# Kernel tuning notes

Hardware: AMD Instinct MI355X
Metric: run time of the kernel (lower is better)

Reference implementation:

```python
import jax, jax.numpy as jnp
import numpy as np
from jax import lax

E = 300      # embed == hidden size
EN_V = 5967  # english vocab
ZH_V = 12016 # chinese vocab
B = 64
S = 64       # max_seq_len


def setup_inputs():
    key = jax.random.key(0)
    ks = jax.random.split(key, 12)
    sc = 1.0 / np.sqrt(E)

    def rn(k, shape):
        return jax.random.normal(k, shape, jnp.float32) * sc

    return {
        "en_input": jax.random.randint(ks[0], (B, S), 0, EN_V),
        "zh_input": jax.random.randint(ks[1], (B, S), 0, ZH_V),
        "en_embed": rn(ks[2], (EN_V, E)),
        "zh_embed": rn(ks[3], (ZH_V, E)),
        "enc_Wih": rn(ks[4], (2, 4 * E, E)),   # layer-stacked, PyTorch gate order i,f,g,o
        "enc_Whh": rn(ks[5], (2, 4 * E, E)),
        "enc_b": rn(ks[6], (2, 4 * E)),        # b_ih + b_hh fused (mathematically identical)
        "dec_Wih": rn(ks[7], (2, 4 * E, E)),
        "dec_Whh": rn(ks[8], (2, 4 * E, E)),
        "dec_b": rn(ks[9], (2, 4 * E)),
        "fc_W": rn(ks[10], (ZH_V, E)),
        "fc_b": rn(ks[11], (ZH_V,)),
    }


def _lstm_layer(x, h0, c0, Wih, Whh, b):
    # x: [B, T, Din]. PyTorch gate order: input, forget, cell(g), output.
    def step(carry, xt):
        h, c = carry
        gates = xt @ Wih.T + h @ Whh.T + b  # [B, 4H]
        i, f, g, o = jnp.split(gates, 4, axis=-1)
        c = jax.nn.sigmoid(f) * c + jax.nn.sigmoid(i) * jnp.tanh(g)
        h = jax.nn.sigmoid(o) * jnp.tanh(c)
        return (h, c), h

    (hT, cT), hs = lax.scan(step, (h0, c0), jnp.swapaxes(x, 0, 1))
    return jnp.swapaxes(hs, 0, 1), hT, cT  # [B,T,H], [B,H], [B,H]


def _lstm2(x, h0, c0, Wih, Whh, b):
    # 2-layer stacked LSTM (dropout between layers disabled: eval-mode math).
    hs, cs = [], []
    out = x
    for l in range(2):
        out, hT, cT = _lstm_layer(out, h0[l], c0[l], Wih[l], Whh[l], b[l])
        hs.append(hT)
        cs.append(cT)
    return out, jnp.stack(hs), jnp.stack(cs)


def reference(en_input, zh_input, en_embed, zh_embed, enc_Wih, enc_Whh, enc_b,
              dec_Wih, dec_Whh, dec_b, fc_W, fc_b):
    zh_feed, zh_target = zh_input[:, :-1], zh_input[:, 1:]
    b = en_input.shape[0]
    z = jnp.zeros((2, b, E), jnp.float32)

    # Encoder over source embeddings; final (h, c) seeds the decoder.
    _, h, c = _lstm2(en_embed[en_input], z, z, enc_Wih, enc_Whh, enc_b)

    # With teaching=True the per-step decoder loop is exactly a full-sequence LSTM.
    dec_out, _, _ = _lstm2(zh_embed[zh_feed], h, c, dec_Wih, dec_Whh, dec_b)

    logits = dec_out @ fc_W.T + fc_b          # [B, S-1, ZH_V]
    log_probs = jax.nn.log_softmax(logits, axis=2)

    # NLL loss with ignore_index=0 (mean over non-pad targets).
    mask = (zh_target != 0).astype(jnp.float32)
    picked = jnp.take_along_axis(log_probs, zh_target[:, :, None], axis=2)[:, :, 0]
    loss = -(picked * mask).sum() / mask.sum()
    return log_probs, loss
```

## Files before the change

kernel.cpp:

```cpp
#include <hip/hip_runtime.h>
#include <stdint.h>

#define EDIM   300
#define EPAD   304
#define KPAD   320
#define NG     1200
#define NB     64
#define SENC   64
#define SDEC   63
#define ZHV    12016
#define DROWS  4032
#define MPAD   4096
#define SENT   0xFFC0ACDCu
#define GSLOT  (NB*NG)

typedef unsigned short u16;
typedef __attribute__((ext_vector_type(8))) short bf16x8;
typedef __attribute__((ext_vector_type(4))) float f32x4;

static __device__ __forceinline__ float bflo(uint32_t u){ return __builtin_bit_cast(float, u << 16); }
static __device__ __forceinline__ float bfhi(uint32_t u){ return __builtin_bit_cast(float, u & 0xffff0000u); }
static __device__ __forceinline__ u16 f2bf(float f){
  uint32_t u = __builtin_bit_cast(uint32_t, f);
  return (u16)((u + 0x7fffu + ((u >> 16) & 1u)) >> 16);
}
static __device__ __forceinline__ float sigm(float x){ return 1.f/(1.f + __expf(-x)); }
static __device__ __forceinline__ float tanhf_(float x){
  x = fminf(fmaxf(x, -15.f), 15.f);
  float e = __expf(2.f*x);
  return (e - 1.f)/(e + 1.f);
}

__global__ void zero_kernel(float4* p, long n){
  long i = (long)blockIdx.x*blockDim.x + threadIdx.x;
  long st = (long)gridDim.x*blockDim.x;
  float4 z = {0.f,0.f,0.f,0.f};
  for (; i < n; i += st) p[i] = z;
}
__global__ void fill_sent(uint32_t* p, long n){
  long i = (long)blockIdx.x*blockDim.x + threadIdx.x;
  long st = (long)gridDim.x*blockDim.x;
  for (; i < n; i += st) p[i] = SENT;
}

__global__ void build_whh(const float* __restrict__ W, u16* __restrict__ out){
  int idx = blockIdx.x*blockDim.x + threadIdx.x;
  if (idx >= 20*38*64) return;
  int jl = idx & 63;
  int kc = (idx >> 6) % 38;
  int g  = (idx >> 6) / 38;
  int G = g/5, w = g - G*5;
  int jg = w*64 + jl;
  union { u16 u[8]; uint4 q; } v;
  for (int e=0;e<8;e++){
    int k = kc*8+e;
    float f = (jg < EDIM && k < EDIM) ? W[(size_t)(G*EDIM + jg)*EDIM + k] : 0.f;
    v.u[e] = f2bf(f);
  }
  ((uint4*)out)[idx] = v.q;
}

__global__ void build_b(const float* __restrict__ W, u16* __restrict__ out, int N){
  int idx = blockIdx.x*blockDim.x + threadIdx.x;
  if (idx >= N*EDIM) return;
  int n = idx / EDIM, k = idx - n*EDIM;
  out[(size_t)n*KPAD + k] = f2bf(W[idx]);
}

__global__ void embed_en(const int* __restrict__ ids, const float* __restrict__ emb, u16* __restrict__ x){
  int idx = blockIdx.x*blockDim.x + threadIdx.x;
  if (idx >= MPAD*EDIM) return;
  int r = idx / EDIM, k = idx - r*EDIM;
  x[(size_t)r*KPAD + k] = f2bf(emb[(size_t)ids[r]*EDIM + k]);
}
__global__ void embed_zh(const int* __restrict__ zh, const float* __restrict__ emb, u16* __restrict__ x){
  int idx = blockIdx.x*blockDim.x + threadIdx.x;
  if (idx >= DROWS*EDIM) return;
  int r = idx / EDIM, k = idx - r*EDIM;
  int b = r / SDEC, t = r - b*SDEC;
  x[(size_t)r*KPAD + k] = f2bf(emb[(size_t)zh[b*SENC + t]*EDIM + k]);
}

#define LDT 40
__global__ __launch_bounds__(256) void gemm_nt(const u16* __restrict__ A, const u16* __restrict__ B,
                float* __restrict__ C, int ldc, int Mreal, int Nreal, const float* __restrict__ bias){
  __shared__ __align__(16) u16 As[128*LDT];
  __shared__ __align__(16) u16 Bs[128*LDT];
  int tid = threadIdx.x;
  int lane = tid & 63, wave = tid >> 6;
  int wm = wave >> 1, wn = wave & 1;
  int m0 = blockIdx.y*128, n0 = blockIdx.x*128;
  f32x4 acc[4][4];
  for (int i=0;i<4;i++) for (int j=0;j<4;j++) acc[i][j] = (f32x4){0.f,0.f,0.f,0.f};
  int r16 = lane & 15, kg = lane >> 4;
  for (int kt=0; kt<KPAD/32; kt++){
    int k0 = kt*32;
    for (int c=0;c<2;c++){
      int id = c*256 + tid;
      int row = id >> 2, col = id & 3;
      *(uint4*)&As[row*LDT + col*8] = *(const uint4*)&A[(size_t)(m0+row)*KPAD + k0 + col*8];
      *(uint4*)&Bs[row*LDT + col*8] = *(const uint4*)&B[(size_t)(n0+row)*KPAD + k0 + col*8];
    }
    __syncthreads();
    bf16x8 af[4], bfr[4];
    for (int i=0;i<4;i++) af[i]  = *(const bf16x8*)&As[(wm*64 + i*16 + r16)*LDT + kg*8];
    for (int j=0;j<4;j++) bfr[j] = *(const bf16x8*)&Bs[(wn*64 + j*16 + r16)*LDT + kg*8];
    for (int i=0;i<4;i++)
      for (int j=0;j<4;j++)
        acc[i][j] = __builtin_amdgcn_mfma_f32_16x16x32_bf16(af[i], bfr[j], acc[i][j], 0, 0, 0);
    __syncthreads();
  }
  for (int j=0;j<4;j++){
    int col = n0 + wn*64 + j*16 + r16;
    if (col >= Nreal) continue;
    float bv = bias ? bias[col] : 0.f;
    for (int i=0;i<4;i++){
      int rbase = m0 + wm*64 + i*16 + kg*4;
      for (int r=0;r<4;r++){
        int row = rbase + r;
        if (row < Mreal) C[(size_t)row*ldc + col] = acc[i][j][r] + bv;
      }
    }
  }
}

__global__ __launch_bounds__(320) void recur_kernel(
    const float* __restrict__ Xih, const u16* __restrict__ Wt,
    const float* __restrict__ bias, const float* __restrict__ h0,
    const float* __restrict__ c0, float* gx,
    u16* seq, float* hfin, float* cfin, int steps)
{
  int r = blockIdx.x >> 2, G = blockIdx.x & 3;
  int tid = threadIdx.x;
  __shared__ __align__(16) float h_lds[EPAD];
  bool act = tid < EDIM;
  int jj = tid;
  int w = jj >> 6, jl = jj & 63;
  int g0 = G*5 + w;
  const uint4* wt4 = (const uint4*)Wt;
  int wbase = g0*38*64 + jl;
  float bj = act ? bias[G*EDIM + jj] : 0.f;
  float c_reg = act ? c0[r*EDIM + tid] : 0.f;
  if (tid < EDIM) h_lds[tid] = h0[r*EDIM + tid];
  else if (tid < EPAD) h_lds[tid] = 0.f;
  __syncthreads();
  int slice0 = G*75;
  for (int t=0; t<steps; t++){
    if (act){
      float xv = Xih[(size_t)(r*steps + t)*NG + G*EDIM + jj];
      float a0=0.f, a1=0.f, a2=0.f, a3=0.f;
      #pragma unroll
      for (int kc=0; kc<38; kc++){
        uint4 wv = wt4[wbase + (kc<<6)];
        float4 hA = *(const float4*)&h_lds[kc*8];
        float4 hB = *(const float4*)&h_lds[kc*8+4];
        a0 += hA.x*bflo(wv.x); a1 += hA.y*bfhi(wv.x);
        a2 += hA.z*bflo(wv.y); a3 += hA.w*bfhi(wv.y);
        a0 += hB.x*bflo(wv.z); a1 += hB.y*bfhi(wv.z);
        a2 += hB.z*bflo(wv.w); a3 += hB.w*bfhi(wv.w);
      }
      float acc = bj + xv + ((a0+a1) + (a2+a3));
      __hip_atomic_store(&gx[(size_t)(t&3)*GSLOT + r*NG + G*EDIM + jj], acc,
                         __ATOMIC_RELAXED, __HIP_MEMORY_SCOPE_AGENT);
    }
    __syncthreads();
    float hv = 0.f;
    if (act){
      const float* g_ = gx + (size_t)(t&3)*GSLOT + r*NG;
      float gi, gf, gg, go;
      for (;;){
        gi = __hip_atomic_load(&g_[tid],          __ATOMIC_RELAXED, __HIP_MEMORY_SCOPE_AGENT);
        gf = __hip_atomic_load(&g_[EDIM + tid],   __ATOMIC_RELAXED, __HIP_MEMORY_SCOPE_AGENT);
        gg = __hip_atomic_load(&g_[2*EDIM + tid], __ATOMIC_RELAXED, __HIP_MEMORY_SCOPE_AGENT);
        go = __hip_atomic_load(&g_[3*EDIM + tid], __ATOMIC_RELAXED, __HIP_MEMORY_SCOPE_AGENT);
        uint32_t ui = __builtin_bit_cast(uint32_t, gi), uf = __builtin_bit_cast(uint32_t, gf);
        uint32_t ug = __builtin_bit_cast(uint32_t, gg), uo = __builtin_bit_cast(uint32_t, go);
        if (ui != SENT && uf != SENT && ug != SENT && uo != SENT) break;
        __builtin_amdgcn_s_sleep(1);
      }
      __hip_atomic_store((uint32_t*)&gx[(size_t)((t+2)&3)*GSLOT + r*NG + G*EDIM + jj], SENT,
                         __ATOMIC_RELAXED, __HIP_MEMORY_SCOPE_AGENT);
      c_reg = sigm(gf)*c_reg + sigm(gi)*tanhf_(gg);
      hv = sigm(go)*tanhf_(c_reg);
      h_lds[tid] = hv;
      if (tid >= slice0 && tid < slice0+75){
        if (seq) seq[(size_t)(r*steps + t)*KPAD + tid] = f2bf(hv);
        if (t == steps-1 && hfin){ hfin[r*EDIM + tid] = hv; cfin[r*EDIM + tid] = c_reg; }
      }
    }
    __syncthreads();
  }
}

__global__ __launch_bounds__(256) void lsm_loss(float* __restrict__ out, const int* __restrict__ zh,
                                                float* __restrict__ lacc){
  int row = blockIdx.x;
  int tid = threadIdx.x;
  __shared__ float buf[ZHV];
  __shared__ float red[8];
  float* p = out + (size_t)row*ZHV;
  float m = -1e30f;
  for (int i=tid; i<ZHV; i+=256){ float v = p[i]; buf[i] = v; m = fmaxf(m, v); }
  for (int off=32; off; off>>=1) m = fmaxf(m, __shfl_xor(m, off));
  if ((tid&63)==0) red[tid>>6] = m;
  __syncthreads();
  m = fmaxf(fmaxf(red[0],red[1]), fmaxf(red[2],red[3]));
  float s = 0.f;
  for (int i=tid; i<ZHV; i+=256) s += __expf(buf[i]-m);
  for (int off=32; off; off>>=1) s += __shfl_xor(s, off);
  if ((tid&63)==0) red[4+(tid>>6)] = s;
  __syncthreads();
  s = red[4]+red[5]+red[6]+red[7];
  float lse = m + __logf(s);
  for (int i=tid; i<ZHV; i+=256) p[i] = buf[i] - lse;
  if (tid == 0){
    int b = row / SDEC, t = row - b*SDEC;
    int tgt = zh[b*SENC + t + 1];
    if (tgt != 0){
      atomicAdd(&lacc[0], -(buf[tgt] - lse));
      atomicAdd(&lacc[1], 1.0f);
    }
  }
}

__global__ void fin_loss(float* out, const float* lacc){
  out[(size_t)DROWS*ZHV] = lacc[0]/lacc[1];
}

extern "C" void kernel_launch(void* const* d_in, const int* in_sizes, int n_in,
                              void* d_out, int out_size, void* d_ws, size_t ws_size,
                              hipStream_t stream){
  const int*   en_in   = (const int*)d_in[0];
  const int*   zh_in   = (const int*)d_in[1];
  const float* en_emb  = (const float*)d_in[2];
  const float* zh_emb  = (const float*)d_in[3];
  const float* enc_Wih = (const float*)d_in[4];
  const float* enc_Whh = (const float*)d_in[5];
  const float* enc_b   = (const float*)d_in[6];
  const float* dec_Wih = (const float*)d_in[7];
  const float* dec_Whh = (const float*)d_in[8];
  const float* dec_b   = (const float*)d_in[9];
  const float* fc_W    = (const float*)d_in[10];
  const float* fc_b    = (const float*)d_in[11];
  float* out = (float*)d_out;
  char* ws = (char*)d_ws;

  size_t o = 0;
  auto alloc = [&](size_t b){ size_t r = o; o = (o + b + 255) & ~(size_t)255; return r; };
  size_t whh[4], wih[4];
  for (int i=0;i<4;i++) whh[i] = alloc((size_t)20*38*64*8*2);
  for (int i=0;i<4;i++) wih[i] = alloc((size_t)1280*KPAD*2);
  size_t fcw  = alloc((size_t)12032*KPAD*2);
  size_t xen  = alloc((size_t)MPAD*KPAD*2);
  size_t xl1e = alloc((size_t)MPAD*KPAD*2);
  size_t xzh  = alloc((size_t)MPAD*KPAD*2);
  size_t xl1d = alloc((size_t)MPAD*KPAD*2);
  size_t xl2d = alloc((size_t)MPAD*KPAD*2);
  size_t xih  = alloc((size_t)MPAD*NG*4);
  size_t gxo  = alloc((size_t)4*4*GSLOT*4);
  size_t hfin = alloc((size_t)2*NB*EDIM*4);
  size_t cfin = alloc((size_t)2*NB*EDIM*4);
  size_t hz   = alloc((size_t)NB*EDIM*4);
  size_t lac  = alloc(256);
  size_t used = o;
  if (ws_size < used) return;

  zero_kernel<<<2048,256,0,stream>>>((float4*)ws, (long)(used/16));
  fill_sent<<<1024,256,0,stream>>>((uint32_t*)(ws+gxo), (long)4*4*GSLOT);

  for (int l=0;l<2;l++){
    build_whh<<<190,256,0,stream>>>(enc_Whh + (size_t)l*NG*EDIM, (u16*)(ws+whh[l]));
    build_whh<<<190,256,0,stream>>>(dec_Whh + (size_t)l*NG*EDIM, (u16*)(ws+whh[2+l]));
    build_b<<<1407,256,0,stream>>>(enc_Wih + (size_t)l*NG*EDIM, (u16*)(ws+wih[l]),   NG);
    build_b<<<1407,256,0,stream>>>(dec_Wih + (size_t)l*NG*EDIM, (u16*)(ws+wih[2+l]), NG);
  }
  build_b<<<(ZHV*EDIM+255)/256,256,0,stream>>>(fc_W, (u16*)(ws+fcw), ZHV);
  embed_en<<<(MPAD*EDIM+255)/256,256,0,stream>>>(en_in, en_emb, (u16*)(ws+xen));
  embed_zh<<<(DROWS*EDIM+255)/256,256,0,stream>>>(zh_in, zh_emb, (u16*)(ws+xzh));

  float* XIH = (float*)(ws+xih);
  float* GX  = (float*)(ws+gxo);
  float* LAC = (float*)(ws+lac);
  float* HF  = (float*)(ws+hfin);
  float* CF  = (float*)(ws+cfin);
  float* HZ  = (float*)(ws+hz);

  gemm_nt<<<dim3(10,32),256,0,stream>>>((u16*)(ws+xen), (u16*)(ws+wih[0]), XIH, NG, MPAD, NG, nullptr);
  recur_kernel<<<256,320,0,stream>>>(XIH, (u16*)(ws+whh[0]), enc_b, HZ, HZ, GX, (u16*)(ws+xl1e), HF, CF, SENC);
  gemm_nt<<<dim3(10,32),256,0,stream>>>((u16*)(ws+xl1e), (u16*)(ws+wih[1]), XIH, NG, MPAD, NG, nullptr);
  recur_kernel<<<256,320,0,stream>>>(XIH, (u16*)(ws+whh[1]), enc_b+NG, HZ, HZ, GX+(size_t)4*GSLOT, nullptr, HF+NB*EDIM, CF+NB*EDIM, SENC);
  gemm_nt<<<dim3(10,32),256,0,stream>>>((u16*)(ws+xzh), (u16*)(ws+wih[2]), XIH, NG, MPAD, NG, nullptr);
  recur_kernel<<<256,320,0,stream>>>(XIH, (u16*)(ws+whh[2]), dec_b, HF, CF, GX+(size_t)8*GSLOT, (u16*)(ws+xl1d), nullptr, nullptr, SDEC);
  gemm_nt<<<dim3(10,32),256,0,stream>>>((u16*)(ws+xl1d), (u16*)(ws+wih[3]), XIH, NG, MPAD, NG, nullptr);
  recur_kernel<<<256,320,0,stream>>>(XIH, (u16*)(ws+whh[3]), dec_b+NG, HF+NB*EDIM, CF+NB*EDIM, GX+(size_t)12*GSLOT, (u16*)(ws+xl2d), nullptr, nullptr, SDEC);
  gemm_nt<<<dim3(94,32),256,0,stream>>>((u16*)(ws+xl2d), (u16*)(ws+fcw), out, ZHV, DROWS, ZHV, fc_b);
  lsm_loss<<<DROWS,256,0,stream>>>(out, zh_in, LAC);
  fin_loss<<<1,1,0,stream>>>(out, LAC);
}
```

Before: 1.728 ms.

## Rewrite LSTM recurrence as register-resident MFMA over five persistent blocks

```diff
diff --git a/kernel.cpp b/kernel.cpp
--- a/kernel.cpp
+++ b/kernel.cpp
@@ -2,7 +2,6 @@
 #include <stdint.h>
 
 #define EDIM   300
-#define EPAD   304
 #define KPAD   320
 #define NG     1200
 #define NB     64
@@ -11,15 +10,13 @@
 #define ZHV    12016
 #define DROWS  4032
 #define MPAD   4096
-#define SENT   0xFFC0ACDCu
-#define GSLOT  (NB*NG)
+#define SENT   0xFFC1FFC1u
+#define HXW    10240
 
 typedef unsigned short u16;
 typedef __attribute__((ext_vector_type(8))) short bf16x8;
 typedef __attribute__((ext_vector_type(4))) float f32x4;
 
-static __device__ __forceinline__ float bflo(uint32_t u){ return __builtin_bit_cast(float, u << 16); }
-static __device__ __forceinline__ float bfhi(uint32_t u){ return __builtin_bit_cast(float, u & 0xffff0000u); }
 static __device__ __forceinline__ u16 f2bf(float f){
   uint32_t u = __builtin_bit_cast(uint32_t, f);
   return (u16)((u + 0x7fffu + ((u >> 16) & 1u)) >> 16);
@@ -43,21 +40,19 @@
   for (; i < n; i += st) p[i] = SENT;
 }
 
-__global__ void build_whh(const float* __restrict__ W, u16* __restrict__ out){
+__global__ void build_wa(const float* __restrict__ W, u16* __restrict__ out){
   int idx = blockIdx.x*blockDim.x + threadIdx.x;
-  if (idx >= 20*38*64) return;
-  int jl = idx & 63;
-  int kc = (idx >> 6) % 38;
-  int g  = (idx >> 6) / 38;
-  int G = g/5, w = g - G*5;
-  int jg = w*64 + jl;
-  union { u16 u[8]; uint4 q; } v;
-  for (int e=0;e<8;e++){
-    int k = kc*8+e;
-    float f = (jg < EDIM && k < EDIM) ? W[(size_t)(G*EDIM + jg)*EDIM + k] : 0.f;
-    v.u[e] = f2bf(f);
-  }
-  ((uint4*)out)[idx] = v.q;
+  if (idx >= 20*4*10*512) return;
+  int e    = idx & 7;
+  int lane = (idx >> 3) & 63;
+  int frag = idx >> 9;
+  int kc = frag % 10;
+  int g  = (frag / 10) & 3;
+  int s  = frag / 40;
+  int j = s*16 + (lane & 15);
+  int k = kc*32 + ((lane >> 4) << 3) + e;
+  float f = (j < EDIM && k < EDIM) ? W[(size_t)(g*EDIM + j)*EDIM + k] : 0.f;
+  out[idx] = f2bf(f);
 }
 
 __global__ void build_b(const float* __restrict__ W, u16* __restrict__ out, int N){
@@ -124,68 +119,130 @@
   }
 }
 
-__global__ __launch_bounds__(320) void recur_kernel(
-    const float* __restrict__ Xih, const u16* __restrict__ Wt,
-    const float* __restrict__ bias, const float* __restrict__ h0,
-    const float* __restrict__ c0, float* gx,
-    u16* seq, float* hfin, float* cfin, int steps)
+__global__ __launch_bounds__(256,1) void recur_mfma(
+    const float* __restrict__ Xih, const u16* __restrict__ WA,
+    const float* __restrict__ h0, const float* __restrict__ c0,
+    uint32_t* hx, u16* seq, float* hfin, float* cfin, int steps)
 {
-  int r = blockIdx.x >> 2, G = blockIdx.x & 3;
   int tid = threadIdx.x;
-  __shared__ __align__(16) float h_lds[EPAD];
-  bool act = tid < EDIM;
-  int jj = tid;
-  int w = jj >> 6, jl = jj & 63;
-  int g0 = G*5 + w;
-  const uint4* wt4 = (const uint4*)Wt;
-  int wbase = g0*38*64 + jl;
-  float bj = act ? bias[G*EDIM + jj] : 0.f;
-  float c_reg = act ? c0[r*EDIM + tid] : 0.f;
-  if (tid < EDIM) h_lds[tid] = h0[r*EDIM + tid];
-  else if (tid < EPAD) h_lds[tid] = 0.f;
+  int lane = tid & 63, wv = tid >> 6;
+  int s = blockIdx.x*4 + wv;
+  int l15 = lane & 15, lk = lane >> 4;
+  int jb = s*16 + lk*4;
+  int jp0 = jb >> 1;
+
+  __shared__ __align__(16) u16 hb[64*KPAD];
+  for (int i = tid; i < 64*KPAD/2; i += 256) ((uint32_t*)hb)[i] = 0;
+
+  bf16x8 wfr[4][10];
+  #pragma unroll
+  for (int g=0; g<4; ++g)
+    #pragma unroll
+    for (int kc=0; kc<10; ++kc)
+      wfr[g][kc] = *(const bf16x8*)&WA[(size_t)((s*4+g)*10 + kc)*512 + lane*8];
+
+  f32x4 creg[4];
+  #pragma unroll
+  for (int nt=0; nt<4; ++nt){
+    int row = nt*16 + l15;
+    float hv4[4];
+    #pragma unroll
+    for (int r=0; r<4; ++r){
+      int j = jb + r;
+      creg[nt][r] = (j < EDIM) ? c0[row*EDIM + j] : 0.f;
+      hv4[r]      = (j < EDIM) ? h0[row*EDIM + j] : 0.f;
+    }
+    uint32_t w0 = (uint32_t)f2bf(hv4[0]) | ((uint32_t)f2bf(hv4[1]) << 16);
+    uint32_t w1 = (uint32_t)f2bf(hv4[2]) | ((uint32_t)f2bf(hv4[3]) << 16);
+    __hip_atomic_store(&hx[3*HXW + jp0*64 + row],     w0, __ATOMIC_RELAXED, __HIP_MEMORY_SCOPE_AGENT);
+    __hip_atomic_store(&hx[3*HXW + (jp0+1)*64 + row], w1, __ATOMIC_RELAXED, __HIP_MEMORY_SCOPE_AGENT);
+  }
   __syncthreads();
-  int slice0 = G*75;
-  for (int t=0; t<steps; t++){
-    if (act){
-      float xv = Xih[(size_t)(r*steps + t)*NG + G*EDIM + jj];
-      float a0=0.f, a1=0.f, a2=0.f, a3=0.f;
-      #pragma unroll
-      for (int kc=0; kc<38; kc++){
-        uint4 wv = wt4[wbase + (kc<<6)];
-        float4 hA = *(const float4*)&h_lds[kc*8];
-        float4 hB = *(const float4*)&h_lds[kc*8+4];
-        a0 += hA.x*bflo(wv.x); a1 += hA.y*bfhi(wv.x);
-        a2 += hA.z*bflo(wv.y); a3 += hA.w*bfhi(wv.y);
-        a0 += hB.x*bflo(wv.z); a1 += hB.y*bfhi(wv.z);
-        a2 += hB.z*bflo(wv.w); a3 += hB.w*bfhi(wv.w);
-      }
-      float acc = bj + xv + ((a0+a1) + (a2+a3));
-      __hip_atomic_store(&gx[(size_t)(t&3)*GSLOT + r*NG + G*EDIM + jj], acc,
-                         __ATOMIC_RELAXED, __HIP_MEMORY_SCOPE_AGENT);
+
+  for (int t=0; t<steps; ++t){
+    int sr = (t+3)&3, sw = t&3, sz = (t+2)&3;
+
+    f32x4 acc[4][4];
+    #pragma unroll
+    for (int g=0; g<4; ++g)
+      #pragma unroll
+      for (int nt=0; nt<4; ++nt){
+        int row = nt*16 + l15;
+        acc[g][nt] = *(const f32x4*)&Xih[(size_t)(row*steps + t)*NG + g*EDIM + jb];
+      }
+
+    {
+      const uint32_t* src = hx + sr*HXW;
+      uint32_t vals[38];
+      #pragma unroll
+      for (int i=0;i<38;++i)
+        vals[i] = __hip_atomic_load(&src[tid + i*256], __ATOMIC_RELAXED, __HIP_MEMORY_SCOPE_AGENT);
+      #pragma unroll
+      for (int i=0;i<38;++i){
+        int w = tid + i*256;
+        while (vals[i] == SENT)
+          vals[i] = __hip_atomic_load(&src[w], __ATOMIC_RELAXED, __HIP_MEMORY_SCOPE_AGENT);
+        int row = w & 63, jp = w >> 6;
+        int u16i = row*KPAD + ((((jp<<2)) ^ ((row&7)<<4)) >> 1);
+        *(uint32_t*)&hb[u16i] = vals[i];
+      }
+    }
+    #pragma unroll
+    for (int nt=0; nt<4; ++nt){
+      int row = nt*16 + l15;
+      __hip_atomic_store(&hx[sz*HXW + jp0*64 + row],     SENT, __ATOMIC_RELAXED, __HIP_MEMORY_SCOPE_AGENT);
+      __hip_atomic_store(&hx[sz*HXW + (jp0+1)*64 + row], SENT, __ATOMIC_RELAXED, __HIP_MEMORY_SCOPE_AGENT);
     }
     __syncthreads();
-    float hv = 0.f;
-    if (act){
-      const float* g_ = gx + (size_t)(t&3)*GSLOT + r*NG;
-      float gi, gf, gg, go;
-      for (;;){
-        gi = __hip_atomic_load(&g_[tid],          __ATOMIC_RELAXED, __HIP_MEMORY_SCOPE_AGENT);
-        gf = __hip_atomic_load(&g_[EDIM + tid],   __ATOMIC_RELAXED, __HIP_MEMORY_SCOPE_AGENT);
-        gg = __hip_atomic_load(&g_[2*EDIM + tid], __ATOMIC_RELAXED, __HIP_MEMORY_SCOPE_AGENT);
-        go = __hip_atomic_load(&g_[3*EDIM + tid], __ATOMIC_RELAXED, __HIP_MEMORY_SCOPE_AGENT);
-        uint32_t ui = __builtin_bit_cast(uint32_t, gi), uf = __builtin_bit_cast(uint32_t, gf);
-        uint32_t ug = __builtin_bit_cast(uint32_t, gg), uo = __builtin_bit_cast(uint32_t, go);
-        if (ui != SENT && uf != SENT && ug != SENT && uo != SENT) break;
-        __builtin_amdgcn_s_sleep(1);
-      }
-      __hip_atomic_store((uint32_t*)&gx[(size_t)((t+2)&3)*GSLOT + r*NG + G*EDIM + jj], SENT,
-                         __ATOMIC_RELAXED, __HIP_MEMORY_SCOPE_AGENT);
-      c_reg = sigm(gf)*c_reg + sigm(gi)*tanhf_(gg);
-      hv = sigm(go)*tanhf_(c_reg);
-      h_lds[tid] = hv;
-      if (tid >= slice0 && tid < slice0+75){
-        if (seq) seq[(size_t)(r*steps + t)*KPAD + tid] = f2bf(hv);
-        if (t == steps-1 && hfin){ hfin[r*EDIM + tid] = hv; cfin[r*EDIM + tid] = c_reg; }
+
+    #pragma unroll
+    for (int kc=0; kc<10; ++kc){
+      bf16x8 hf[4];
+      #pragma unroll
+      for (int nt=0; nt<4; ++nt){
+        int row = nt*16 + l15;
+        int kbyte = kc*64 + (lk<<4);
+        hf[nt] = *(const bf16x8*)&hb[row*KPAD + ((kbyte ^ ((row&7)<<4)) >> 1)];
+      }
+      #pragma unroll
+      for (int g=0; g<4; ++g)
+        #pragma unroll
+        for (int nt=0; nt<4; ++nt)
+          acc[g][nt] = __builtin_amdgcn_mfma_f32_16x16x32_bf16(wfr[g][kc], hf[nt], acc[g][nt], 0, 0, 0);
+    }
+
+    #pragma unroll
+    for (int nt=0; nt<4; ++nt){
+      int row = nt*16 + l15;
+      float hv4[4];
+      #pragma unroll
+      for (int r=0; r<4; ++r){
+        float gi = acc[0][nt][r], gf = acc[1][nt][r];
+        float gg = acc[2][nt][r], go = acc[3][nt][r];
+        float c = sigm(gf)*creg[nt][r] + sigm(gi)*tanhf_(gg);
+        creg[nt][r] = c;
+        hv4[r] = sigm(go)*tanhf_(c);
+      }
+      uint32_t w0 = (uint32_t)f2bf(hv4[0]) | ((uint32_t)f2bf(hv4[1]) << 16);
+      uint32_t w1 = (uint32_t)f2bf(hv4[2]) | ((uint32_t)f2bf(hv4[3]) << 16);
+      __hip_atomic_store(&hx[sw*HXW + jp0*64 + row],     w0, __ATOMIC_RELAXED, __HIP_MEMORY_SCOPE_AGENT);
+      __hip_atomic_store(&hx[sw*HXW + (jp0+1)*64 + row], w1, __ATOMIC_RELAXED, __HIP_MEMORY_SCOPE_AGENT);
+      if (seq){
+        size_t sb = (size_t)(row*steps + t)*KPAD + jb;
+        if (jb + 3 < EDIM){
+          uint2 q; q.x = w0; q.y = w1;
+          *(uint2*)&seq[sb] = q;
+        } else {
+          #pragma unroll
+          for (int r=0; r<4; ++r) if (jb + r < EDIM) seq[sb + r] = f2bf(hv4[r]);
+        }
+      }
+      if (t == steps-1 && hfin){
+        #pragma unroll
+        for (int r=0; r<4; ++r) if (jb + r < EDIM){
+          hfin[row*EDIM + jb + r] = hv4[r];
+          cfin[row*EDIM + jb + r] = creg[nt][r];
+        }
       }
     }
     __syncthreads();
@@ -247,8 +304,8 @@
 
   size_t o = 0;
   auto alloc = [&](size_t b){ size_t r = o; o = (o + b + 255) & ~(size_t)255; return r; };
-  size_t whh[4], wih[4];
-  for (int i=0;i<4;i++) whh[i] = alloc((size_t)20*38*64*8*2);
+  size_t wa[4], wih[4];
+  for (int i=0;i<4;i++) wa[i]  = alloc((size_t)20*4*10*512*2);
   for (int i=0;i<4;i++) wih[i] = alloc((size_t)1280*KPAD*2);
   size_t fcw  = alloc((size_t)12032*KPAD*2);
   size_t xen  = alloc((size_t)MPAD*KPAD*2);
@@ -256,8 +313,8 @@
   size_t xzh  = alloc((size_t)MPAD*KPAD*2);
   size_t xl1d = alloc((size_t)MPAD*KPAD*2);
   size_t xl2d = alloc((size_t)MPAD*KPAD*2);
-  size_t xih  = alloc((size_t)MPAD*NG*4);
-  size_t gxo  = alloc((size_t)4*4*GSLOT*4);
+  size_t xih  = alloc(((size_t)MPAD*NG + 64)*4);
+  size_t hxo  = alloc((size_t)4*4*HXW*4);
   size_t hfin = alloc((size_t)2*NB*EDIM*4);
   size_t cfin = alloc((size_t)2*NB*EDIM*4);
   size_t hz   = alloc((size_t)NB*EDIM*4);
@@ -266,11 +323,11 @@
   if (ws_size < used) return;
 
   zero_kernel<<<2048,256,0,stream>>>((float4*)ws, (long)(used/16));
-  fill_sent<<<1024,256,0,stream>>>((uint32_t*)(ws+gxo), (long)4*4*GSLOT);
+  fill_sent<<<1024,256,0,stream>>>((uint32_t*)(ws+hxo), (long)4*4*HXW);
 
   for (int l=0;l<2;l++){
-    build_whh<<<190,256,0,stream>>>(enc_Whh + (size_t)l*NG*EDIM, (u16*)(ws+whh[l]));
-    build_whh<<<190,256,0,stream>>>(dec_Whh + (size_t)l*NG*EDIM, (u16*)(ws+whh[2+l]));
+    build_wa<<<1600,256,0,stream>>>(enc_Whh + (size_t)l*NG*EDIM, (u16*)(ws+wa[l]));
+    build_wa<<<1600,256,0,stream>>>(dec_Whh + (size_t)l*NG*EDIM, (u16*)(ws+wa[2+l]));
     build_b<<<1407,256,0,stream>>>(enc_Wih + (size_t)l*NG*EDIM, (u16*)(ws+wih[l]),   NG);
     build_b<<<1407,256,0,stream>>>(dec_Wih + (size_t)l*NG*EDIM, (u16*)(ws+wih[2+l]), NG);
   }
@@ -279,20 +336,20 @@
   embed_zh<<<(DROWS*EDIM+255)/256,256,0,stream>>>(zh_in, zh_emb, (u16*)(ws+xzh));
 
   float* XIH = (float*)(ws+xih);
-  float* GX  = (float*)(ws+gxo);
+  uint32_t* HX = (uint32_t*)(ws+hxo);
   float* LAC = (float*)(ws+lac);
   float* HF  = (float*)(ws+hfin);
   float* CF  = (float*)(ws+cfin);
   float* HZ  = (float*)(ws+hz);
 
-  gemm_nt<<<dim3(10,32),256,0,stream>>>((u16*)(ws+xen), (u16*)(ws+wih[0]), XIH, NG, MPAD, NG, nullptr);
-  recur_kernel<<<256,320,0,stream>>>(XIH, (u16*)(ws+whh[0]), enc_b, HZ, HZ, GX, (u16*)(ws+xl1e), HF, CF, SENC);
-  gemm_nt<<<dim3(10,32),256,0,stream>>>((u16*)(ws+xl1e), (u16*)(ws+wih[1]), XIH, NG, MPAD, NG, nullptr);
-  recur_kernel<<<256,320,0,stream>>>(XIH, (u16*)(ws+whh[1]), enc_b+NG, HZ, HZ, GX+(size_t)4*GSLOT, nullptr, HF+NB*EDIM, CF+NB*EDIM, SENC);
-  gemm_nt<<<dim3(10,32),256,0,stream>>>((u16*)(ws+xzh), (u16*)(ws+wih[2]), XIH, NG, MPAD, NG, nullptr);
-  recur_kernel<<<256,320,0,stream>>>(XIH, (u16*)(ws+whh[2]), dec_b, HF, CF, GX+(size_t)8*GSLOT, (u16*)(ws+xl1d), nullptr, nullptr, SDEC);
-  gemm_nt<<<dim3(10,32),256,0,stream>>>((u16*)(ws+xl1d), (u16*)(ws+wih[3]), XIH, NG, MPAD, NG, nullptr);
-  recur_kernel<<<256,320,0,stream>>>(XIH, (u16*)(ws+whh[3]), dec_b+NG, HF+NB*EDIM, CF+NB*EDIM, GX+(size_t)12*GSLOT, (u16*)(ws+xl2d), nullptr, nullptr, SDEC);
+  gemm_nt<<<dim3(10,32),256,0,stream>>>((u16*)(ws+xen), (u16*)(ws+wih[0]), XIH, NG, MPAD, NG, enc_b);
+  recur_mfma<<<5,256,0,stream>>>(XIH, (u16*)(ws+wa[0]), HZ, HZ, HX, (u16*)(ws+xl1e), HF, CF, SENC);
+  gemm_nt<<<dim3(10,32),256,0,stream>>>((u16*)(ws+xl1e), (u16*)(ws+wih[1]), XIH, NG, MPAD, NG, enc_b+NG);
+  recur_mfma<<<5,256,0,stream>>>(XIH, (u16*)(ws+wa[1]), HZ, HZ, HX+(size_t)4*HXW, nullptr, HF+NB*EDIM, CF+NB*EDIM, SENC);
+  gemm_nt<<<dim3(10,32),256,0,stream>>>((u16*)(ws+xzh), (u16*)(ws+wih[2]), XIH, NG, MPAD, NG, dec_b);
+  recur_mfma<<<5,256,0,stream>>>(XIH, (u16*)(ws+wa[2]), HF, CF, HX+(size_t)8*HXW, (u16*)(ws+xl1d), nullptr, nullptr, SDEC);
+  gemm_nt<<<dim3(10,32),256,0,stream>>>((u16*)(ws+xl1d), (u16*)(ws+wih[3]), XIH, NG, MPAD, NG, dec_b+NG);
+  recur_mfma<<<5,256,0,stream>>>(XIH, (u16*)(ws+wa[3]), HF+NB*EDIM, CF+NB*EDIM, HX+(size_t)12*HXW, (u16*)(ws+xl2d), nullptr, nullptr, SDEC);
   gemm_nt<<<dim3(94,32),256,0,stream>>>((u16*)(ws+xl2d), (u16*)(ws+fcw), out, ZHV, DROWS, ZHV, fc_b);
   lsm_loss<<<DROWS,256,0,stream>>>(out, zh_in, LAC);
   fin_loss<<<1,1,0,stream>>>(out, LAC);
```

Measured after the change: 2.381 ms. 37.8% more time.
